# Optimization experiments

Hardware: AMD Instinct MI355X
Metric: run time of the kernel (lower is better)

The kernel has to match this reference:

```python
import jax, jax.numpy as jnp
import numpy as np
import math

B, T, F, H, C = 64, 128, 2048, 1024, 22

def setup_inputs() -> dict:
    key = jax.random.key(0)
    ks = jax.random.split(key, 16)
    def w(k, shape, fan_in):
        s = 1.0 / math.sqrt(fan_in)
        return jax.random.uniform(k, shape, jnp.float32, -s, s)
    return {
        "x": jax.random.normal(ks[0], (B, T, F), jnp.float32),
        # encoder LSTM (input F, hidden H); PyTorch gate order i,f,g,o
        "enc_Wih": w(ks[1], (4 * H, F), H),
        "enc_Whh": w(ks[2], (4 * H, H), H),
        "enc_bih": w(ks[3], (4 * H,), H),
        "enc_bhh": w(ks[4], (4 * H,), H),
        # enc->dec and dec->enc projections (both HxH, unidirectional)
        "We2d": w(ks[5], (H, H), H),
        "be2d": w(ks[6], (H,), H),
        "Wd2e": w(ks[7], (H, H), H),
        "bd2e": w(ks[8], (H,), H),
        # decoder LSTMCell (input F + H, hidden H)
        "dec_Wih": w(ks[9], (4 * H, F + H), H),
        "dec_Whh": w(ks[10], (4 * H, H), H),
        "dec_bih": w(ks[11], (4 * H,), H),
        "dec_bhh": w(ks[12], (4 * H,), H),
        # classifier
        "Wc": w(ks[13], (C, H), H),
        "bc": w(ks[14], (C,), H),
    }

def _lstm_cell(x_t, h, c, Wih, Whh, b):
    g = x_t @ Wih.T + h @ Whh.T + b  # [B, 4H]
    i, f, gg, o = jnp.split(g, 4, axis=-1)
    c_new = jax.nn.sigmoid(f) * c + jax.nn.sigmoid(i) * jnp.tanh(gg)
    h_new = jax.nn.sigmoid(o) * jnp.tanh(c_new)
    return h_new, c_new

def reference(x, enc_Wih, enc_Whh, enc_bih, enc_bhh, We2d, be2d, Wd2e, bd2e,
              dec_Wih, dec_Whh, dec_bih, dec_bhh, Wc, bc):
    Bx, Tx, _ = x.shape
    Hh = enc_Whh.shape[1]
    enc_b = enc_bih + enc_bhh
    dec_b = dec_bih + dec_bhh

    # ---- encoder LSTM over time (feature extractor is identity) ----
    xT = jnp.swapaxes(x, 0, 1)  # [T, B, F]
    def enc_step(carry, x_t):
        h, c = carry
        h, c = _lstm_cell(x_t, h, c, enc_Wih, enc_Whh, enc_b)
        return (h, c), h
    h0 = jnp.zeros((Bx, Hh), x.dtype)
    (_, _), h_ts = jax.lax.scan(enc_step, (h0, h0), xT)  # [T, B, H]
    h_ts = jnp.swapaxes(h_ts, 0, 1)  # [B, T, H]

    proj_h_ts = h_ts @ We2d.T + be2d  # [B, T, H]
    scale = 1.0 / math.sqrt(Hh)

    # ---- decoder with per-step attention ----
    def dec_step(carry, x_t):
        h, c = carry
        logits = jnp.einsum('bh,bth->bt', h, proj_h_ts) * scale
        aw = jax.nn.softmax(logits, axis=-1)           # [B, T]
        attn = jnp.einsum('bt,bth->bh', aw, proj_h_ts)  # [B, H]
        attn = attn @ Wd2e.T + bd2e
        inp = jnp.concatenate([x_t, attn], axis=-1)     # [B, F+H]
        h, c = _lstm_cell(inp, h, c, dec_Wih, dec_Whh, dec_b)
        sc = h @ Wc.T + bc                              # [B, C]
        return (h, c), (sc, aw)

    (_, _), (scores_T, aw_T) = jax.lax.scan(dec_step, (h0, h0), xT)
    scores = jnp.swapaxes(scores_T, 0, 1)  # [B, T, C]
    return scores, aw_T[-1]  # last step's attention weights [B, T]
```

## Files before the change

### kernel.cpp

```cpp
#include <hip/hip_runtime.h>
#include <hip/hip_bf16.h>

#define BB 64
#define TT 128
#define FF 2048
#define HH 1024
#define CC 22
#define G4 4096
#define KD 2048
#define BT 8192

typedef __attribute__((ext_vector_type(8))) short bf16x8;
typedef __attribute__((ext_vector_type(4))) float f32x4;

__device__ __forceinline__ f32x4 mfma16(bf16x8 a, bf16x8 b, f32x4 c) {
    return __builtin_amdgcn_mfma_f32_16x16x32_bf16(a, b, c, 0, 0, 0);
}

__device__ __forceinline__ float b2f(short s) {
    unsigned int u = ((unsigned int)(unsigned short)s) << 16;
    union { unsigned int i; float f; } x; x.i = u; return x.f;
}

__device__ __forceinline__ short f2bs(float f) {
    union { __hip_bfloat16 h; short s; } u;
    u.h = __float2bfloat16(f);
    return u.s;
}


__global__ void zero_u32(unsigned int* p, long long n) {
    long long i = (long long)blockIdx.x * 256 + threadIdx.x;
    if (i < n) p[i] = 0u;
}

__global__ void fill_f32(float* p, long long n, float v) {
    long long i = (long long)blockIdx.x * 256 + threadIdx.x;
    if (i < n) p[i] = v;
}

__global__ void pack_bf16(const float* __restrict__ src, long long sld, long long soff,
                          __hip_bfloat16* __restrict__ dst, long long dld,
                          int rows, int cols, int valid) {
    long long i = (long long)blockIdx.x * 256 + threadIdx.x;
    long long tot = (long long)rows * cols;
    if (i >= tot) return;
    int r = (int)(i / cols), c = (int)(i % cols);
    float v = (r < valid) ? src[(long long)r * sld + soff + c] : 0.f;
    dst[(long long)r * dld + c] = __float2bfloat16(v);
}

__global__ void packT_bf16(const float* __restrict__ src, int R, int Ccols,
                           __hip_bfloat16* __restrict__ dst) {
    long long i = (long long)blockIdx.x * 256 + threadIdx.x;
    long long tot = (long long)R * Ccols;
    if (i >= tot) return;
    int r = (int)(i / Ccols), c = (int)(i % Ccols);
    dst[(long long)c * R + r] = __float2bfloat16(src[i]);
}

__global__ void add_bias2(const float* a, const float* b, float* out, int n) {
    int i = blockIdx.x * 256 + threadIdx.x;
    if (i < n) out[i] = a[i] + b[i];
}

__global__ void pad_bias(const float* src, float* dst, int nsrc, int ndst) {
    int i = blockIdx.x * blockDim.x + threadIdx.x;
    if (i < ndst) dst[i] = (i < nsrc) ? src[i] : 0.f;
}

__global__ __launch_bounds__(64) void bcomb_kernel(const float* __restrict__ dWih,
                                                   const float* __restrict__ bd2e,
                                                   const float* __restrict__ dbih,
                                                   const float* __restrict__ dbhh,
                                                   float* __restrict__ badd) {
    int r = blockIdx.x, lane = threadIdx.x;
    const float* row = dWih + (long long)r * (FF + HH) + FF;
    float s = 0.f;
    for (int k = lane; k < HH; k += 64) s += row[k] * bd2e[k];
    #pragma unroll
    for (int off = 32; off; off >>= 1) s += __shfl_xor(s, off, 64);
    if (lane == 0) badd[r] = s + dbih[r] + dbhh[r];
}

template <int K, bool AF32>
__global__ __launch_bounds__(256) void gemm_tile(
    const void* __restrict__ Aptr, long long lda,
    const __hip_bfloat16* __restrict__ W,
    const float* __restrict__ bias, void* __restrict__ Cout, int out_bf16,
    long long ldc, int n_store) {
    int tid = threadIdx.x;
    int wave = tid >> 6, lane = tid & 63;
    int wm = wave >> 1, wn = wave & 1;
    int m_base = blockIdx.x * 128 + wm * 64;
    int n_base = blockIdx.y * 128 + wn * 64;
    int row_in = lane & 15, k8 = (lane >> 4) * 8;

    f32x4 acc[4][4] = {};
    const float* Af = (const float*)Aptr + (long long)(m_base + row_in) * lda + k8;
    const __hip_bfloat16* Ab = (const __hip_bfloat16*)Aptr + (long long)(m_base + row_in) * lda + k8;
    const __hip_bfloat16* Wp = W + (long long)(n_base + row_in) * K + k8;

    #pragma unroll 2
    for (int k0 = 0; k0 < K; k0 += 32) {
        bf16x8 a[4], b[4];
        #pragma unroll
        for (int i = 0; i < 4; i++) {
            if (AF32) {
                const float* p = Af + (long long)i * 16 * lda + k0;
                #pragma unroll
                for (int j = 0; j < 8; j++) a[i][j] = f2bs(p[j]);
            } else {
                a[i] = *(const bf16x8*)(Ab + (long long)i * 16 * lda + k0);
            }
        }
        #pragma unroll
        for (int i = 0; i < 4; i++) b[i] = *(const bf16x8*)(Wp + (long long)i * 16 * K + k0);
        #pragma unroll
        for (int mt = 0; mt < 4; mt++)
            #pragma unroll
            for (int nt = 0; nt < 4; nt++)
                acc[mt][nt] = mfma16(a[mt], b[nt], acc[mt][nt]);
    }

    int col = lane & 15, rowq = (lane >> 4) * 4;
    #pragma unroll
    for (int mt = 0; mt < 4; mt++)
        #pragma unroll
        for (int nt = 0; nt < 4; nt++) {
            int n = n_base + nt * 16 + col;
            if (n >= n_store) continue;
            float bv = bias ? bias[n] : 0.f;
            #pragma unroll
            for (int r = 0; r < 4; r++) {
                long long m = m_base + mt * 16 + rowq + r;
                float v = acc[mt][nt][r] + bv;
                if (out_bf16) ((__hip_bfloat16*)Cout)[m * ldc + n] = __float2bfloat16(v);
                else          ((float*)Cout)[m * ldc + n] = v;
            }
        }
}

template <int KZ>
__global__ __launch_bounds__(1024) void fused_step(
    const __hip_bfloat16* __restrict__ Z,
    const __hip_bfloat16* __restrict__ W,
    const __hip_bfloat16* __restrict__ Xg_t, long long xg_stride,
    float* __restrict__ c,
    float* __restrict__ h_f32,
    __hip_bfloat16* __restrict__ hb_a, long long stride_a,
    __hip_bfloat16* __restrict__ hb_b, long long stride_b) {
    constexpr int KQ = KZ / 4;
    __shared__ float P[16 * 256];
    int tid = threadIdx.x;
    int wave = tid >> 6, lane = tid & 63;
    int g = wave >> 2, ks = wave & 3;
    int hh_t = blockIdx.x & 63, mb = blockIdx.x >> 6;
    int m_base = mb * 16;
    int hh0 = hh_t * 16;
    int n0 = g * HH + hh0;
    int row_in = lane & 15, k8 = (lane >> 4) * 8;
    long long koff = (long long)ks * KQ + k8;

    const __hip_bfloat16* Ap = Z + (long long)(m_base + row_in) * KZ + koff;
    const __hip_bfloat16* Wp = W + (long long)(n0 + row_in) * KZ + koff;

    f32x4 acc = {};
    #pragma unroll 4
    for (int k0 = 0; k0 < KQ; k0 += 32) {
        bf16x8 bw = *(const bf16x8*)(Wp + k0);
        bf16x8 a0 = *(const bf16x8*)(Ap + k0);
        acc = mfma16(a0, bw, acc);
    }

    int col = lane & 15, rowq = (lane >> 4) * 4;
    #pragma unroll
    for (int r = 0; r < 4; r++)
        P[wave * 256 + (rowq + r) * 16 + col] = acc[r];
    __syncthreads();

    if (tid < 256) {
        int bl = tid >> 4, hl = tid & 15;
        int bb = m_base + bl, hh = hh0 + hl;
        float gv[4];
        #pragma unroll
        for (int gg2 = 0; gg2 < 4; gg2++) {
            float s = 0.f;
            #pragma unroll
            for (int kk = 0; kk < 4; kk++) s += P[(gg2 * 4 + kk) * 256 + tid];
            gv[gg2] = s + __bfloat162float(Xg_t[(long long)bb * xg_stride + gg2 * HH + hh]);
        }
        float si = 1.f / (1.f + __expf(-gv[0]));
        float sf = 1.f / (1.f + __expf(-gv[1]));
        float tg = tanhf(gv[2]);
        float so = 1.f / (1.f + __expf(-gv[3]));
        long long idx = (long long)bb * HH + hh;
        float cn = sf * c[idx] + si * tg;
        c[idx] = cn;
        float hn = so * tanhf(cn);
        if (h_f32) h_f32[idx] = hn;
        __hip_bfloat16 hb = __float2bfloat16(hn);
        hb_a[(long long)bb * stride_a + hh] = hb;
        hb_b[(long long)bb * stride_b + hh] = hb;
    }
}

__global__ __launch_bounds__(1024) void attention_k(
    const float* __restrict__ h_dec,
    const __hip_bfloat16* __restrict__ proj,
    __hip_bfloat16* __restrict__ Z,
    float* __restrict__ aw_out) {
    __shared__ float osum[16][1024];
    __shared__ float logits[TT];
    __shared__ float red[2];
    int b = blockIdx.x;
    int tid = threadIdx.x, wave = tid >> 6, lane = tid & 63;

    float hreg[16];
    const float* hp = h_dec + (long long)b * HH + lane * 16;
    #pragma unroll
    for (int j = 0; j < 16; j++) hreg[j] = hp[j];

    const __hip_bfloat16* pb = proj + (long long)b * TT * HH + lane * 16;
    const float scale = 0.03125f;

    #pragma unroll
    for (int i = 0; i < 8; i++) {
        int t = wave + i * 16;
        const __hip_bfloat16* p = pb + (long long)t * HH;
        bf16x8 p0 = *(const bf16x8*)(p);
        bf16x8 p1 = *(const bf16x8*)(p + 8);
        float dot = 0.f;
        #pragma unroll
        for (int j = 0; j < 8; j++) dot += hreg[j] * b2f(p0[j]) + hreg[8 + j] * b2f(p1[j]);
        #pragma unroll
        for (int off = 32; off; off >>= 1) dot += __shfl_xor(dot, off, 64);
        if (lane == 0) logits[t] = dot * scale;
    }
    __syncthreads();

    if (wave == 0) {
        float a = logits[lane], c2 = logits[lane + 64];
        float mx = fmaxf(a, c2);
        #pragma unroll
        for (int off = 32; off; off >>= 1) mx = fmaxf(mx, __shfl_xor(mx, off, 64));
        float s = __expf(a - mx) + __expf(c2 - mx);
        #pragma unroll
        for (int off = 32; off; off >>= 1) s += __shfl_xor(s, off, 64);
        if (lane == 0) { red[0] = mx; red[1] = s; }
    }
    __syncthreads();
    float mstar = red[0], invL = 1.f / red[1];

    float o[16];
    #pragma unroll
    for (int j = 0; j < 16; j++) o[j] = 0.f;
    #pragma unroll
    for (int i = 0; i < 8; i++) {
        int t = wave + i * 16;
        float w = __expf(logits[t] - mstar);
        const __hip_bfloat16* p = pb + (long long)t * HH;
        bf16x8 p0 = *(const bf16x8*)(p);
        bf16x8 p1 = *(const bf16x8*)(p + 8);
        #pragma unroll
        for (int j = 0; j < 8; j++) { o[j] += w * b2f(p0[j]); o[8 + j] += w * b2f(p1[j]); }
    }
    #pragma unroll
    for (int j = 0; j < 16; j++) osum[wave][j * 64 + lane] = o[j];
    __syncthreads();

    float s = 0.f;
    #pragma unroll
    for (int w = 0; w < 16; w++) s += osum[w][tid];
    int q = (tid & 63) * 16 + (tid >> 6);
    Z[(long long)b * KD + q] = __float2bfloat16(s * invL);

    if (aw_out && tid < TT)
        aw_out[(long long)b * TT + tid] = __expf(logits[tid] - mstar) * invL;
}


extern "C" void kernel_launch(void* const* d_in, const int* in_sizes, int n_in,
                              void* d_out, int out_size, void* d_ws, size_t ws_size,
                              hipStream_t stream) {
    const float* x    = (const float*)d_in[0];
    const float* eWih = (const float*)d_in[1];
    const float* eWhh = (const float*)d_in[2];
    const float* ebih = (const float*)d_in[3];
    const float* ebhh = (const float*)d_in[4];
    const float* We2d = (const float*)d_in[5];
    const float* be2d = (const float*)d_in[6];
    const float* Wd2e = (const float*)d_in[7];
    const float* bd2e = (const float*)d_in[8];
    const float* dWih = (const float*)d_in[9];
    const float* dWhh = (const float*)d_in[10];
    const float* dbih = (const float*)d_in[11];
    const float* dbhh = (const float*)d_in[12];
    const float* Wc   = (const float*)d_in[13];
    const float* bc   = (const float*)d_in[14];

    float* scores = (float*)d_out;
    float* aw_out = scores + (size_t)BB * TT * CC;

    char* ws = (char*)d_ws;
    size_t off = 0;
    auto alloc = [&](size_t bytes) -> char* {
        char* p = ws + off;
        off = (off + bytes + 255) & ~(size_t)255;
        return p;
    };

    __hip_bfloat16* Xg    = (__hip_bfloat16*)alloc((size_t)BT * G4 * 2);
    char*           Bz    = alloc((size_t)G4 * KD * 2);
    char*           Cp    = alloc((size_t)G4 * FF * 2);
    __hip_bfloat16* hts   = (__hip_bfloat16*)alloc((size_t)BT * HH * 2);
    __hip_bfloat16* Wd2eT = (__hip_bfloat16*)alloc((size_t)HH * HH * 2);
    __hip_bfloat16* We2dB = (__hip_bfloat16*)alloc((size_t)HH * HH * 2);
    __hip_bfloat16* WcP   = (__hip_bfloat16*)alloc((size_t)128 * HH * 2);
    float*          encb  = (float*)alloc((size_t)G4 * 4);
    float*          badd  = (float*)alloc((size_t)G4 * 4);
    float*          bcP   = (float*)alloc((size_t)128 * 4);
    char*           state = alloc(1572864);
    float*          cenc = (float*)(state);
    float*          cdec = (float*)(state + 262144);
    float*          hdec = (float*)(state + 524288);
    __hip_bfloat16* he0  = (__hip_bfloat16*)(state + 786432);
    __hip_bfloat16* he1  = (__hip_bfloat16*)(state + 917504);
    __hip_bfloat16* Zb0  = (__hip_bfloat16*)(state + 1048576);
    __hip_bfloat16* Zb1  = (__hip_bfloat16*)(state + 1310720);

    __hip_bfloat16* eWhhB = (__hip_bfloat16*)Bz;
    __hip_bfloat16* Wz    = (__hip_bfloat16*)Bz;
    __hip_bfloat16* eWihB = (__hip_bfloat16*)Cp;
    __hip_bfloat16* dWxB  = (__hip_bfloat16*)Cp;
    __hip_bfloat16* proj  = (__hip_bfloat16*)Cp;
    __hip_bfloat16* hdts  = hts;

    (void)in_sizes; (void)n_in;

    if (off > ws_size) {
        long long n = out_size;
        fill_f32<<<dim3((unsigned)((n + 255) / 256)), 256, 0, stream>>>((float*)d_out, n, 111.0f);
        return;
    }

    auto packGrid = [](long long tot) { return dim3((unsigned)((tot + 255) / 256)); };

    zero_u32<<<dim3(1536), dim3(256), 0, stream>>>((unsigned int*)state, 393216LL);
    pack_bf16<<<packGrid((long long)G4 * FF), 256, 0, stream>>>(eWih, FF, 0, eWihB, FF, G4, FF, G4);
    pack_bf16<<<packGrid((long long)G4 * HH), 256, 0, stream>>>(eWhh, HH, 0, eWhhB, HH, G4, HH, G4);
    packT_bf16<<<packGrid((long long)HH * HH), 256, 0, stream>>>(Wd2e, HH, HH, Wd2eT);
    pack_bf16<<<packGrid((long long)HH * HH), 256, 0, stream>>>(We2d, HH, 0, We2dB, HH, HH, HH, HH);
    pack_bf16<<<packGrid((long long)128 * HH), 256, 0, stream>>>(Wc, HH, 0, WcP, HH, 128, HH, CC);
    add_bias2<<<16, 256, 0, stream>>>(ebih, ebhh, encb, G4);
    pad_bias<<<1, 128, 0, stream>>>(bc, bcP, CC, 128);
    bcomb_kernel<<<G4, 64, 0, stream>>>(dWih, bd2e, dbih, dbhh, badd);

    gemm_tile<FF, true><<<dim3(BT / 128, G4 / 128), 256, 0, stream>>>(
        x, FF, eWihB, encb, Xg, 1, G4, G4);

    for (int t = 0; t < TT; t++) {
        __hip_bfloat16* hin  = (t & 1) ? he1 : he0;
        __hip_bfloat16* hout = (t & 1) ? he0 : he1;
        fused_step<HH><<<dim3(256), dim3(1024), 0, stream>>>(
            hin, eWhhB, Xg + (size_t)t * G4, (long long)TT * G4,
            cenc, nullptr, hout, HH, hts + (size_t)t * HH, (long long)TT * HH);
    }

    pack_bf16<<<packGrid((long long)G4 * FF), 256, 0, stream>>>(dWih, FF + HH, 0, dWxB, FF, G4, FF, G4);
    gemm_tile<FF, true><<<dim3(BT / 128, G4 / 128), 256, 0, stream>>>(
        x, FF, dWxB, badd, Xg, 1, G4, G4);

    gemm_tile<HH, true><<<dim3(G4 / 128, HH / 128), 256, 0, stream>>>(
        dWih + FF, FF + HH, Wd2eT, nullptr, Wz, 1, KD, HH);
    pack_bf16<<<packGrid((long long)G4 * HH), 256, 0, stream>>>(dWhh, HH, 0, Wz + HH, KD, G4, HH, G4);

    gemm_tile<HH, false><<<dim3(BT / 128, HH / 128), 256, 0, stream>>>(
        hts, HH, We2dB, be2d, proj, 1, HH, HH);

    for (int t = 0; t < TT; t++) {
        __hip_bfloat16* Zin  = (t & 1) ? Zb1 : Zb0;
        __hip_bfloat16* Znxt = (t & 1) ? Zb0 : Zb1;
        attention_k<<<dim3(BB), dim3(1024), 0, stream>>>(
            hdec, proj, Zin, (t == TT - 1) ? aw_out : nullptr);
        fused_step<KD><<<dim3(256), dim3(1024), 0, stream>>>(
            Zin, Wz, Xg + (size_t)t * G4, (long long)TT * G4,
            cdec, hdec, Znxt + HH, KD, hdts + (size_t)t * HH, (long long)TT * HH);
    }

    gemm_tile<HH, false><<<dim3(BT / 128, 1), 256, 0, stream>>>(
        hdts, HH, WcP, bcP, scores, 0, CC, CC);
}
```

Measured before the change: 6.734 ms.

## Fuse decoder attention into LSTM step kernel with per-batch flag sync

```diff
diff --git a/kernel.cpp b/kernel.cpp
--- a/kernel.cpp
+++ b/kernel.cpp
@@ -26,6 +26,14 @@
     union { __hip_bfloat16 h; short s; } u;
     u.h = __float2bfloat16(f);
     return u.s;
+}
+
+__device__ __forceinline__ bf16x8 loadA16_agent(const __hip_bfloat16* p) {
+    union { unsigned long long u[2]; bf16x8 v; } x;
+    const unsigned long long* q = (const unsigned long long*)p;
+    x.u[0] = __hip_atomic_load(q,     __ATOMIC_RELAXED, __HIP_MEMORY_SCOPE_AGENT);
+    x.u[1] = __hip_atomic_load(q + 1, __ATOMIC_RELAXED, __HIP_MEMORY_SCOPE_AGENT);
+    return x.v;
 }
 
 
@@ -108,8 +116,12 @@
         for (int i = 0; i < 4; i++) {
             if (AF32) {
                 const float* p = Af + (long long)i * 16 * lda + k0;
-                #pragma unroll
-                for (int j = 0; j < 8; j++) a[i][j] = f2bs(p[j]);
+                const float4 f0 = *(const float4*)(p);
+                const float4 f1 = *(const float4*)(p + 4);
+                a[i][0] = f2bs(f0.x); a[i][1] = f2bs(f0.y);
+                a[i][2] = f2bs(f0.z); a[i][3] = f2bs(f0.w);
+                a[i][4] = f2bs(f1.x); a[i][5] = f2bs(f1.y);
+                a[i][6] = f2bs(f1.z); a[i][7] = f2bs(f1.w);
             } else {
                 a[i] = *(const bf16x8*)(Ab + (long long)i * 16 * lda + k0);
             }
@@ -166,7 +178,7 @@
     const __hip_bfloat16* Wp = W + (long long)(n0 + row_in) * KZ + koff;
 
     f32x4 acc = {};
-    #pragma unroll 4
+    #pragma unroll 8
     for (int k0 = 0; k0 < KQ; k0 += 32) {
         bf16x8 bw = *(const bf16x8*)(Wp + k0);
         bf16x8 a0 = *(const bf16x8*)(Ap + k0);
@@ -205,14 +217,15 @@
     }
 }
 
-__global__ __launch_bounds__(1024) void attention_k(
+__device__ __forceinline__ void attn_body(
+    float* __restrict__ smem,
     const float* __restrict__ h_dec,
     const __hip_bfloat16* __restrict__ proj,
     __hip_bfloat16* __restrict__ Z,
     float* __restrict__ aw_out) {
-    __shared__ float osum[16][1024];
-    __shared__ float logits[TT];
-    __shared__ float red[2];
+    float* osum   = smem;
+    float* logits = smem + 16 * 1024;
+    float* red    = logits + TT;
     int b = blockIdx.x;
     int tid = threadIdx.x, wave = tid >> 6, lane = tid & 63;
 
@@ -266,17 +279,103 @@
         for (int j = 0; j < 8; j++) { o[j] += w * b2f(p0[j]); o[8 + j] += w * b2f(p1[j]); }
     }
     #pragma unroll
-    for (int j = 0; j < 16; j++) osum[wave][j * 64 + lane] = o[j];
+    for (int j = 0; j < 16; j++) osum[wave * 1024 + j * 64 + lane] = o[j];
     __syncthreads();
 
     float s = 0.f;
     #pragma unroll
-    for (int w = 0; w < 16; w++) s += osum[w][tid];
+    for (int w = 0; w < 16; w++) s += osum[w * 1024 + tid];
     int q = (tid & 63) * 16 + (tid >> 6);
     Z[(long long)b * KD + q] = __float2bfloat16(s * invL);
 
     if (aw_out && tid < TT)
         aw_out[(long long)b * TT + tid] = __expf(logits[tid] - mstar) * invL;
+}
+
+__global__ __launch_bounds__(1024) void dec_step(
+    const float* __restrict__ hdec_in,
+    const __hip_bfloat16* __restrict__ proj,
+    __hip_bfloat16* __restrict__ Zin,
+    const __hip_bfloat16* __restrict__ Wz,
+    const __hip_bfloat16* __restrict__ Xg_t, long long xg_stride,
+    float* __restrict__ c, float* __restrict__ hdec_out,
+    __hip_bfloat16* __restrict__ Znxt_h,
+    __hip_bfloat16* __restrict__ hdts_t,
+    unsigned int* __restrict__ flags, unsigned int want,
+    float* __restrict__ aw_out) {
+    __shared__ float smem[16 * 1024 + TT + 2];
+    int tid = threadIdx.x;
+    int bx = blockIdx.x;
+
+    if (bx < BB) {
+        attn_body(smem, hdec_in, proj, Zin, aw_out);
+        __syncthreads();
+        if (tid == 0)
+            __hip_atomic_store(&flags[bx], want, __ATOMIC_RELEASE, __HIP_MEMORY_SCOPE_AGENT);
+    }
+
+    float* P = smem;
+    int wave = tid >> 6, lane = tid & 63;
+    int g = wave >> 2, ks = wave & 3;
+    int hh_t = bx & 63, mb = bx >> 6;
+    int m_base = mb * 16, hh0 = hh_t * 16, n0 = g * HH + hh0;
+    int row_in = lane & 15, k8 = (lane >> 4) * 8;
+    long long koff = (long long)ks * 512 + k8;
+
+    const __hip_bfloat16* Ap = Zin + (long long)(m_base + row_in) * KD + koff;
+    const __hip_bfloat16* Wp = Wz + (long long)(n0 + row_in) * KD + koff;
+
+    f32x4 acc = {};
+    if (ks >= 2) {
+        #pragma unroll 8
+        for (int k0 = 0; k0 < 512; k0 += 32) {
+            bf16x8 bw = *(const bf16x8*)(Wp + k0);
+            bf16x8 a0 = *(const bf16x8*)(Ap + k0);
+            acc = mfma16(a0, bw, acc);
+        }
+    } else {
+        const unsigned int* fp = flags + m_base + row_in;
+        while (__hip_atomic_load(fp, __ATOMIC_RELAXED, __HIP_MEMORY_SCOPE_AGENT) < want)
+            __builtin_amdgcn_s_sleep(2);
+        asm volatile("" ::: "memory");
+        #pragma unroll 8
+        for (int k0 = 0; k0 < 512; k0 += 32) {
+            bf16x8 bw = *(const bf16x8*)(Wp + k0);
+            bf16x8 a0 = loadA16_agent(Ap + k0);
+            acc = mfma16(a0, bw, acc);
+        }
+    }
+
+    int col = lane & 15, rowq = (lane >> 4) * 4;
+    #pragma unroll
+    for (int r = 0; r < 4; r++)
+        P[wave * 256 + (rowq + r) * 16 + col] = acc[r];
+    __syncthreads();
+
+    if (tid < 256) {
+        int bl = tid >> 4, hl = tid & 15;
+        int bb = m_base + bl, hh = hh0 + hl;
+        float gv[4];
+        #pragma unroll
+        for (int gg2 = 0; gg2 < 4; gg2++) {
+            float s = 0.f;
+            #pragma unroll
+            for (int kk = 0; kk < 4; kk++) s += P[(gg2 * 4 + kk) * 256 + tid];
+            gv[gg2] = s + __bfloat162float(Xg_t[(long long)bb * xg_stride + gg2 * HH + hh]);
+        }
+        float si = 1.f / (1.f + __expf(-gv[0]));
+        float sf = 1.f / (1.f + __expf(-gv[1]));
+        float tg = tanhf(gv[2]);
+        float so = 1.f / (1.f + __expf(-gv[3]));
+        long long idx = (long long)bb * HH + hh;
+        float cn = sf * c[idx] + si * tg;
+        c[idx] = cn;
+        float hn = so * tanhf(cn);
+        hdec_out[idx] = hn;
+        __hip_bfloat16 hb = __float2bfloat16(hn);
+        Znxt_h[(long long)bb * KD + hh] = hb;
+        hdts_t[(long long)bb * (TT * HH) + hh] = hb;
+    }
 }
 
 
@@ -320,7 +419,7 @@
     float*          encb  = (float*)alloc((size_t)G4 * 4);
     float*          badd  = (float*)alloc((size_t)G4 * 4);
     float*          bcP   = (float*)alloc((size_t)128 * 4);
-    char*           state = alloc(1572864);
+    char*           state = alloc(1572864 + 256);
     float*          cenc = (float*)(state);
     float*          cdec = (float*)(state + 262144);
     float*          hdec = (float*)(state + 524288);
@@ -328,6 +427,7 @@
     __hip_bfloat16* he1  = (__hip_bfloat16*)(state + 917504);
     __hip_bfloat16* Zb0  = (__hip_bfloat16*)(state + 1048576);
     __hip_bfloat16* Zb1  = (__hip_bfloat16*)(state + 1310720);
+    unsigned int*   dflags = (unsigned int*)(state + 1572864);
 
     __hip_bfloat16* eWhhB = (__hip_bfloat16*)Bz;
     __hip_bfloat16* Wz    = (__hip_bfloat16*)Bz;
@@ -346,7 +446,7 @@
 
     auto packGrid = [](long long tot) { return dim3((unsigned)((tot + 255) / 256)); };
 
-    zero_u32<<<dim3(1536), dim3(256), 0, stream>>>((unsigned int*)state, 393216LL);
+    zero_u32<<<dim3(1537), dim3(256), 0, stream>>>((unsigned int*)state, 393280LL);
     pack_bf16<<<packGrid((long long)G4 * FF), 256, 0, stream>>>(eWih, FF, 0, eWihB, FF, G4, FF, G4);
     pack_bf16<<<packGrid((long long)G4 * HH), 256, 0, stream>>>(eWhh, HH, 0, eWhhB, HH, G4, HH, G4);
     packT_bf16<<<packGrid((long long)HH * HH), 256, 0, stream>>>(Wd2e, HH, HH, Wd2eT);
@@ -381,11 +481,10 @@
     for (int t = 0; t < TT; t++) {
         __hip_bfloat16* Zin  = (t & 1) ? Zb1 : Zb0;
         __hip_bfloat16* Znxt = (t & 1) ? Zb0 : Zb1;
-        attention_k<<<dim3(BB), dim3(1024), 0, stream>>>(
-            hdec, proj, Zin, (t == TT - 1) ? aw_out : nullptr);
-        fused_step<KD><<<dim3(256), dim3(1024), 0, stream>>>(
-            Zin, Wz, Xg + (size_t)t * G4, (long long)TT * G4,
-            cdec, hdec, Znxt + HH, KD, hdts + (size_t)t * HH, (long long)TT * HH);
+        dec_step<<<dim3(256), dim3(1024), 0, stream>>>(
+            hdec, proj, Zin, Wz, Xg + (size_t)t * G4, (long long)TT * G4,
+            cdec, hdec, Znxt + HH, hdts + (size_t)t * HH,
+            dflags, (unsigned)(t + 1), (t == TT - 1) ? aw_out : nullptr);
     }
 
     gemm_tile<HH, false><<<dim3(BT / 128, 1), 256, 0, stream>>>(
```

After: 7.637 ms. 1.13x slower.

## Split decoder attention into logits and weighted-sum kernels across more blocks

Applied to the files above, without the earlier changes.

```diff
diff --git a/kernel.cpp b/kernel.cpp
--- a/kernel.cpp
+++ b/kernel.cpp
@@ -108,8 +108,12 @@
         for (int i = 0; i < 4; i++) {
             if (AF32) {
                 const float* p = Af + (long long)i * 16 * lda + k0;
-                #pragma unroll
-                for (int j = 0; j < 8; j++) a[i][j] = f2bs(p[j]);
+                const float4 f0 = *(const float4*)(p);
+                const float4 f1 = *(const float4*)(p + 4);
+                a[i][0] = f2bs(f0.x); a[i][1] = f2bs(f0.y);
+                a[i][2] = f2bs(f0.z); a[i][3] = f2bs(f0.w);
+                a[i][4] = f2bs(f1.x); a[i][5] = f2bs(f1.y);
+                a[i][6] = f2bs(f1.z); a[i][7] = f2bs(f1.w);
             } else {
                 a[i] = *(const bf16x8*)(Ab + (long long)i * 16 * lda + k0);
             }
@@ -166,7 +170,7 @@
     const __hip_bfloat16* Wp = W + (long long)(n0 + row_in) * KZ + koff;
 
     f32x4 acc = {};
-    #pragma unroll 4
+    #pragma unroll 8
     for (int k0 = 0; k0 < KQ; k0 += 32) {
         bf16x8 bw = *(const bf16x8*)(Wp + k0);
         bf16x8 a0 = *(const bf16x8*)(Ap + k0);
@@ -205,15 +209,12 @@
     }
 }
 
-__global__ __launch_bounds__(1024) void attention_k(
+__global__ __launch_bounds__(1024) void logits_k(
     const float* __restrict__ h_dec,
     const __hip_bfloat16* __restrict__ proj,
-    __hip_bfloat16* __restrict__ Z,
-    float* __restrict__ aw_out) {
-    __shared__ float osum[16][1024];
-    __shared__ float logits[TT];
-    __shared__ float red[2];
-    int b = blockIdx.x;
+    float* __restrict__ logits_g) {
+    int bx = blockIdx.x;
+    int b = bx & 63, tq = bx >> 6;
     int tid = threadIdx.x, wave = tid >> 6, lane = tid & 63;
 
     float hreg[16];
@@ -225,8 +226,8 @@
     const float scale = 0.03125f;
 
     #pragma unroll
-    for (int i = 0; i < 8; i++) {
-        int t = wave + i * 16;
+    for (int it = 0; it < 2; it++) {
+        int t = tq * 32 + wave * 2 + it;
         const __hip_bfloat16* p = pb + (long long)t * HH;
         bf16x8 p0 = *(const bf16x8*)(p);
         bf16x8 p1 = *(const bf16x8*)(p + 8);
@@ -235,12 +236,27 @@
         for (int j = 0; j < 8; j++) dot += hreg[j] * b2f(p0[j]) + hreg[8 + j] * b2f(p1[j]);
         #pragma unroll
         for (int off = 32; off; off >>= 1) dot += __shfl_xor(dot, off, 64);
-        if (lane == 0) logits[t] = dot * scale;
-    }
+        if (lane == 0) logits_g[b * TT + t] = dot * scale;
+    }
+}
+
+__global__ __launch_bounds__(1024) void attnsum_k(
+    const float* __restrict__ logits_g,
+    const __hip_bfloat16* __restrict__ proj,
+    __hip_bfloat16* __restrict__ Z,
+    float* __restrict__ aw_out) {
+    __shared__ float lsm[TT];
+    __shared__ float red[2];
+    __shared__ float osum[32 * 264];
+    int bx = blockIdx.x;
+    int b = bx & 63, hq = bx >> 6;
+    int tid = threadIdx.x, wave = tid >> 6, lane = tid & 63;
+
+    if (tid < TT) lsm[tid] = logits_g[b * TT + tid];
     __syncthreads();
 
     if (wave == 0) {
-        float a = logits[lane], c2 = logits[lane + 64];
+        float a = lsm[lane], c2 = lsm[lane + 64];
         float mx = fmaxf(a, c2);
         #pragma unroll
         for (int off = 32; off; off >>= 1) mx = fmaxf(mx, __shfl_xor(mx, off, 64));
@@ -252,31 +268,31 @@
     __syncthreads();
     float mstar = red[0], invL = 1.f / red[1];
 
-    float o[16];
-    #pragma unroll
-    for (int j = 0; j < 16; j++) o[j] = 0.f;
-    #pragma unroll
-    for (int i = 0; i < 8; i++) {
-        int t = wave + i * 16;
-        float w = __expf(logits[t] - mstar);
-        const __hip_bfloat16* p = pb + (long long)t * HH;
-        bf16x8 p0 = *(const bf16x8*)(p);
-        bf16x8 p1 = *(const bf16x8*)(p + 8);
-        #pragma unroll
-        for (int j = 0; j < 8; j++) { o[j] += w * b2f(p0[j]); o[8 + j] += w * b2f(p1[j]); }
-    }
-    #pragma unroll
-    for (int j = 0; j < 16; j++) osum[wave][j * 64 + lane] = o[j];
+    int hw = tid & 31, tg = tid >> 5;
+    const __hip_bfloat16* base = proj + (long long)b * TT * HH + hq * 256 + hw * 8;
+    float o8[8];
+    #pragma unroll
+    for (int j = 0; j < 8; j++) o8[j] = 0.f;
+    #pragma unroll
+    for (int k = 0; k < 4; k++) {
+        int t = tg + k * 32;
+        float w = __expf(lsm[t] - mstar) * invL;
+        bf16x8 p = *(const bf16x8*)(base + (long long)t * HH);
+        #pragma unroll
+        for (int j = 0; j < 8; j++) o8[j] += w * b2f(p[j]);
+    }
+    #pragma unroll
+    for (int j = 0; j < 8; j++) osum[tg * 264 + hw * 8 + j] = o8[j];
     __syncthreads();
 
-    float s = 0.f;
-    #pragma unroll
-    for (int w = 0; w < 16; w++) s += osum[w][tid];
-    int q = (tid & 63) * 16 + (tid >> 6);
-    Z[(long long)b * KD + q] = __float2bfloat16(s * invL);
-
-    if (aw_out && tid < TT)
-        aw_out[(long long)b * TT + tid] = __expf(logits[tid] - mstar) * invL;
+    if (tid < 256) {
+        float s = 0.f;
+        #pragma unroll
+        for (int g2 = 0; g2 < 32; g2++) s += osum[g2 * 264 + tid];
+        Z[(long long)b * KD + hq * 256 + tid] = __float2bfloat16(s);
+    }
+    if (aw_out && hq == 0 && tid < TT)
+        aw_out[(long long)b * TT + tid] = __expf(lsm[tid] - mstar) * invL;
 }
 
 
@@ -320,7 +336,7 @@
     float*          encb  = (float*)alloc((size_t)G4 * 4);
     float*          badd  = (float*)alloc((size_t)G4 * 4);
     float*          bcP   = (float*)alloc((size_t)128 * 4);
-    char*           state = alloc(1572864);
+    char*           state = alloc(1572864 + 32768);
     float*          cenc = (float*)(state);
     float*          cdec = (float*)(state + 262144);
     float*          hdec = (float*)(state + 524288);
@@ -328,6 +344,7 @@
     __hip_bfloat16* he1  = (__hip_bfloat16*)(state + 917504);
     __hip_bfloat16* Zb0  = (__hip_bfloat16*)(state + 1048576);
     __hip_bfloat16* Zb1  = (__hip_bfloat16*)(state + 1310720);
+    float*          logits_g = (float*)(state + 1572864);
 
     __hip_bfloat16* eWhhB = (__hip_bfloat16*)Bz;
     __hip_bfloat16* Wz    = (__hip_bfloat16*)Bz;
@@ -381,8 +398,9 @@
     for (int t = 0; t < TT; t++) {
         __hip_bfloat16* Zin  = (t & 1) ? Zb1 : Zb0;
         __hip_bfloat16* Znxt = (t & 1) ? Zb0 : Zb1;
-        attention_k<<<dim3(BB), dim3(1024), 0, stream>>>(
-            hdec, proj, Zin, (t == TT - 1) ? aw_out : nullptr);
+        logits_k<<<dim3(256), dim3(1024), 0, stream>>>(hdec, proj, logits_g);
+        attnsum_k<<<dim3(256), dim3(1024), 0, stream>>>(
+            logits_g, proj, Zin, (t == TT - 1) ? aw_out : nullptr);
         fused_step<KD><<<dim3(256), dim3(1024), 0, stream>>>(
             Zin, Wz, Xg + (size_t)t * G4, (long long)TT * G4,
             cdec, hdec, Znxt + HH, KD, hdts + (size_t)t * HH, (long long)TT * HH);
```

Result: faster. 6.310 ms (-6.3%).
